# Kernel optimization log

Measured on AMD Instinct MI355X. Metric: run time of the kernel, lower is better.

## Reference

```python
import jax, jax.numpy as jnp
import numpy as np

EPS_SUM = 1e-8   # matches tf divide epsilon on column sums
EPS_L2 = 1e-12   # tf.nn.l2_normalize default epsilon inside CosineSimilarity
EPS_LOG = 1e-8


def _l2norm_rows(x):
    # rows: (k, N); matches tf.nn.l2_normalize(x, axis=-1)
    sq = jnp.sum(x * x, axis=-1, keepdims=True)
    return x * jax.lax.rsqrt(jnp.maximum(sq, EPS_L2))


def setup_inputs() -> dict:
    key = jax.random.key(0)
    k0, k1 = jax.random.split(key)
    N, K = 200000, 256
    c_0 = jax.random.uniform(k0, (N, K), dtype=jnp.float32)
    c_1 = jax.random.uniform(k1, (N, K), dtype=jnp.float32)
    return {"c_0": c_0, "c_1": c_1, "k": K}


def reference(c_0, c_1, k):
    # --- cluster-size entropy terms ---
    s0 = jnp.sum(c_0, axis=0)                      # (k,)
    s1 = jnp.sum(c_1, axis=0)
    p_0 = s0 / jnp.sum(s0)
    p_1 = s1 / jnp.sum(s1)
    log_k = jnp.log(jnp.float32(k))
    entrpy_loss = (jnp.sum(p_0 * jnp.log(p_0)) + log_k) + \
                  (jnp.sum(p_1 * jnp.log(p_1)) + log_k)

    # --- column-sum normalize, transpose to (k, N) ---
    c0n = (c_0 / (s0[None, :] + EPS_SUM)).T        # (k, N)
    c1n = (c_1 / (s1[None, :] + EPS_SUM)).T        # (k, N)

    # cosine similarity matrix via row L2-normalization + small GEMM
    a = _l2norm_rows(c0n)                          # (k, N)
    b = _l2norm_rows(c1n)                          # (k, N)
    c_smi = jnp.einsum('kn,jn->kj', a, b)          # (k, k) cosine sims

    diag = jnp.diagonal(jax.nn.softmax(c_smi, axis=-1))  # (k,)
    cls_loss = -jnp.mean(jnp.log(diag + EPS_LOG))
    return (cls_loss, entrpy_loss)
```

## Files before the change

### kernel.cpp

```cpp
#include <hip/hip_runtime.h>
#include <hip/hip_bf16.h>

typedef __attribute__((ext_vector_type(4))) float f32x4;
typedef __attribute__((ext_vector_type(4))) int   i32x4;
typedef __attribute__((ext_vector_type(8))) short s16x8;

#define KCOLS 256
#define KC 32

__device__ __forceinline__ int swz_idx(int col, int koct){
    return ((col >> 1) << 6) + ((((((col & 1) << 2) | koct)) ^ ((col >> 2) & 7)) << 3);
}

__device__ __forceinline__ int cvt2(float lo, float hi){
    int r;
    asm("v_cvt_pk_bf16_f32 %0, %1, %2" : "=v"(r) : "v"(lo), "v"(hi));
    return r;
}

__device__ __forceinline__ void block_barrier(){
    asm volatile("s_waitcnt lgkmcnt(0)" ::: "memory");
    __builtin_amdgcn_sched_barrier(0);
    __builtin_amdgcn_s_barrier();
    __builtin_amdgcn_sched_barrier(0);
    asm volatile("" ::: "memory");
}

__global__ __launch_bounds__(512, 2) void k1_gemm(
        const float* __restrict__ c0, const float* __restrict__ c1,
        float* __restrict__ Pc, float* __restrict__ Ps, int nrows)
{
    const int tid = threadIdx.x;
    const int w   = tid >> 6;
    const int l   = tid & 63;
    const int mat = w >> 2;
    const int oct = w & 3;
    const int wr  = w >> 2;
    const int wc  = w & 3;
    const int b   = blockIdx.x;
    const int B   = gridDim.x;
    const int nchunk = (nrows + KC - 1) / KC;

    __shared__ __align__(16) unsigned short lds[2][2][8192];
    __shared__ float sred[2][4][256];
    __shared__ float qred[2][4][256];

    const float* src = mat ? c1 : c0;
    const int colbase = l << 2;

    int idxA[8], idxB[4];
#pragma unroll
    for (int mt = 0; mt < 8; ++mt)
        idxA[mt] = swz_idx(wr*128 + mt*16 + (l & 15), l >> 4);
#pragma unroll
    for (int nt = 0; nt < 4; ++nt)
        idxB[nt] = swz_idx(wc*64 + nt*16 + (l & 15), l >> 4);

    int widx[4];
#pragma unroll
    for (int cc = 0; cc < 4; ++cc)
        widx[cc] = (((l << 1) + (cc >> 1)) << 6) +
                   ((((((cc & 1) << 2) | oct)) ^ (l & 7)) << 3);

    f32x4 acc[8][4];
    const f32x4 zf = {0.f, 0.f, 0.f, 0.f};
#pragma unroll
    for (int i = 0; i < 8; ++i)
#pragma unroll
        for (int j = 0; j < 4; ++j) acc[i][j] = zf;

    float sum[4] = {0.f,0.f,0.f,0.f};
    float sq [4] = {0.f,0.f,0.f,0.f};

    f32x4 f[8];
    auto LOAD = [&](int c){
        int rbase = c*KC + oct*8;
        if (rbase + 8 <= nrows){
#pragma unroll
            for (int rr = 0; rr < 8; ++rr)
                f[rr] = *(const f32x4*)(src + (size_t)(rbase+rr)*KCOLS + colbase);
        } else {
#pragma unroll
            for (int rr = 0; rr < 8; ++rr){
                int row = rbase + rr;
                f[rr] = (row < nrows) ? *(const f32x4*)(src + (size_t)row*KCOLS + colbase) : zf;
            }
        }
    };

    int c = b;
    if (c < nchunk) LOAD(c);
    int p = 0;
    while (c < nchunk){
        unsigned short* dst = &lds[p][mat][0];
#pragma unroll
        for (int cc = 0; cc < 4; ++cc){
            float v0=f[0][cc], v1=f[1][cc], v2=f[2][cc], v3=f[3][cc];
            float v4=f[4][cc], v5=f[5][cc], v6=f[6][cc], v7=f[7][cc];
            sum[cc] += ((v0+v1)+(v2+v3)) + ((v4+v5)+(v6+v7));
            sq [cc] += ((v0*v0+v1*v1)+(v2*v2+v3*v3)) + ((v4*v4+v5*v5)+(v6*v6+v7*v7));
            i32x4 pk;
            pk.x = cvt2(v0, v1);
            pk.y = cvt2(v2, v3);
            pk.z = cvt2(v4, v5);
            pk.w = cvt2(v6, v7);
            *(i32x4*)&dst[widx[cc]] = pk;
        }

        int cn = c + B;
        if (cn < nchunk) LOAD(cn);

        block_barrier();

        const unsigned short* bufA = &lds[p][0][0];
        const unsigned short* bufB = &lds[p][1][0];
        s16x8 bfr[4];
#pragma unroll
        for (int nt = 0; nt < 4; ++nt) bfr[nt] = *(const s16x8*)&bufB[idxB[nt]];
#pragma unroll
        for (int mt = 0; mt < 8; ++mt){
            s16x8 afr = *(const s16x8*)&bufA[idxA[mt]];
#pragma unroll
            for (int nt = 0; nt < 4; ++nt)
                acc[mt][nt] = __builtin_amdgcn_mfma_f32_16x16x32_bf16(
                                  afr, bfr[nt], acc[mt][nt], 0, 0, 0);
        }
        p ^= 1;
        c  = cn;
    }

    float* Pb = Pc + (size_t)b * 65536;
#pragma unroll
    for (int mt = 0; mt < 8; ++mt)
#pragma unroll
        for (int nt = 0; nt < 4; ++nt)
#pragma unroll
            for (int r = 0; r < 4; ++r){
                int row = wr*128 + mt*16 + (l >> 4)*4 + r;
                int cl  = wc*64  + nt*16 + (l & 15);
                Pb[row*256 + cl] = acc[mt][nt][r];
            }

#pragma unroll
    for (int cc = 0; cc < 4; ++cc){
        sred[mat][oct][colbase + cc] = sum[cc];
        qred[mat][oct][colbase + cc] = sq[cc];
    }
    __syncthreads();
    {
        int m2 = tid >> 8, cl = tid & 255;
        float s = sred[m2][0][cl] + sred[m2][1][cl] + sred[m2][2][cl] + sred[m2][3][cl];
        float q = qred[m2][0][cl] + qred[m2][1][cl] + qred[m2][2][cl] + qred[m2][3][cl];
        Ps[(size_t)b*1024 + m2*512 + cl]       = s;
        Ps[(size_t)b*1024 + m2*512 + 256 + cl] = q;
    }
}

__global__ __launch_bounds__(256) void k2_sum(const float* __restrict__ Ps,
                                              float* __restrict__ fin, int B)
{
    int tid = threadIdx.x;
    int u   = blockIdx.x*64 + (tid & 63);
    int sub = tid >> 6;
    double a = 0.0;
    for (int b = sub; b < B; b += 4) a += Ps[(size_t)b*1024 + u];
    __shared__ double sc2[4][64];
    sc2[sub][tid & 63] = a;
    __syncthreads();
    if (sub == 0)
        fin[u] = (float)(sc2[0][tid] + sc2[1][tid] + sc2[2][tid] + sc2[3][tid]);
}

__global__ __launch_bounds__(512) void k3_rows(const float* __restrict__ Pc,
        const float* __restrict__ fin, float* __restrict__ tout, int B)
{
    const int j   = blockIdx.x;
    const int tid = threadIdx.x;
    const int l   = tid & 255;
    const int h   = tid >> 8;

    __shared__ float part[2][256];
    __shared__ float cosS[256];
    __shared__ float wred[8];

    double a = 0.0;
    int b0 = h ? (B >> 1) : 0;
    int b1 = h ? B        : (B >> 1);
    for (int b = b0; b < b1; ++b)
        a += Pc[(size_t)b*65536 + j*256 + l];
    part[h][l] = (float)a;
    __syncthreads();

    if (h == 0){
        float Cjl = part[0][l] + part[1][l];
        float d0 = fin[j]       + 1e-8f, q0 = fin[256 + j];
        float d1 = fin[512 + l] + 1e-8f, q1 = fin[768 + l];
        float rs0 = rsqrtf(fmaxf(q0 / (d0*d0), 1e-12f));
        float rs1 = rsqrtf(fmaxf(q1 / (d1*d1), 1e-12f));
        cosS[l] = Cjl * (rs0 / d0) * (rs1 / d1);
    }
    __syncthreads();

    float v  = (tid < 256) ? cosS[tid] : -3.0e38f;
    float mx = v;
#pragma unroll
    for (int o = 32; o >= 1; o >>= 1) mx = fmaxf(mx, __shfl_xor(mx, o));
    if ((tid & 63) == 0) wred[tid >> 6] = mx;
    __syncthreads();
    mx = wred[0];
#pragma unroll
    for (int i = 1; i < 8; ++i) mx = fmaxf(mx, wred[i]);
    __syncthreads();

    float e = (tid < 256) ? expf(cosS[tid] - mx) : 0.0f;
    float s = e;
#pragma unroll
    for (int o = 32; o >= 1; o >>= 1) s += __shfl_xor(s, o);
    if ((tid & 63) == 0) wred[tid >> 6] = s;
    __syncthreads();
    float S = ((wred[0]+wred[1])+(wred[2]+wred[3])) + ((wred[4]+wred[5])+(wred[6]+wred[7]));

    if (tid == j){
        float dg = expf(cosS[j] - mx) / S;
        tout[j] = logf(dg + 1e-8f);
    }
}

__global__ __launch_bounds__(256) void k4_fin(const float* __restrict__ fin,
        const float* __restrict__ tout, const int* __restrict__ kptr,
        float* __restrict__ out)
{
    const int tid = threadIdx.x;
    __shared__ double sc[4];
    auto bsum = [&](double v) -> double {
#pragma unroll
        for (int o = 32; o >= 1; o >>= 1) v += __shfl_xor(v, o);
        if ((tid & 63) == 0) sc[tid >> 6] = v;
        __syncthreads();
        double r = sc[0] + sc[1] + sc[2] + sc[3];
        __syncthreads();
        return r;
    };

    double s0 = fin[tid], s1 = fin[512 + tid];
    double S0 = bsum(s0), S1 = bsum(s1);
    double p0 = s0 / S0, p1 = s1 / S1;
    double T0 = bsum(p0 * log(p0));
    double T1 = bsum(p1 * log(p1));
    double Tc = bsum((double)tout[tid]);

    if (tid == 0){
        double lk = log((double)(*kptr));
        out[0] = (float)(-(Tc / 256.0));
        out[1] = (float)((T0 + lk) + (T1 + lk));
    }
}

extern "C" void kernel_launch(void* const* d_in, const int* in_sizes, int n_in,
                              void* d_out, int out_size, void* d_ws, size_t ws_size,
                              hipStream_t stream)
{
    const float* c0  = (const float*)d_in[0];
    const float* c1  = (const float*)d_in[1];
    const int*  kptr = (const int*)d_in[2];
    float* out = (float*)d_out;
    int nrows = in_sizes[0] / KCOLS;

    int B = 250;
    size_t need = ((size_t)B*66560 + 1280) * sizeof(float);
    if (need > ws_size){
        long cap = (long)(ws_size / sizeof(float)) - 1280;
        long bb  = cap / 66560;
        B = (int)(bb < 1 ? 1 : (bb > 250 ? 250 : bb));
    }
    float* Pc  = (float*)d_ws;
    float* Ps  = Pc + (size_t)B * 65536;
    float* fin = Ps + (size_t)B * 1024;
    float* tv  = fin + 1024;

    hipLaunchKernelGGL(k1_gemm, dim3(B),   dim3(512), 0, stream, c0, c1, Pc, Ps, nrows);
    hipLaunchKernelGGL(k2_sum,  dim3(16),  dim3(256), 0, stream, Ps, fin, B);
    hipLaunchKernelGGL(k3_rows, dim3(256), dim3(512), 0, stream, Pc, fin, tv, B);
    hipLaunchKernelGGL(k4_fin,  dim3(1),   dim3(256), 0, stream, fin, tv, kptr, out);
}
```

Measured before the change: 144.8 us.

## Stream inputs via async global-to-LDS DMA ring with triple buffering

```diff
diff --git a/kernel.cpp b/kernel.cpp
--- a/kernel.cpp
+++ b/kernel.cpp
@@ -2,6 +2,7 @@
 #include <hip/hip_bf16.h>
 
 typedef __attribute__((ext_vector_type(4))) float f32x4;
+typedef __attribute__((ext_vector_type(2))) int   i32x2;
 typedef __attribute__((ext_vector_type(4))) int   i32x4;
 typedef __attribute__((ext_vector_type(8))) short s16x8;
 
@@ -18,35 +19,37 @@
     return r;
 }
 
-__device__ __forceinline__ void block_barrier(){
-    asm volatile("s_waitcnt lgkmcnt(0)" ::: "memory");
-    __builtin_amdgcn_sched_barrier(0);
-    __builtin_amdgcn_s_barrier();
-    __builtin_amdgcn_sched_barrier(0);
-    asm volatile("" ::: "memory");
-}
+__device__ __forceinline__ void dma16(const float* g, float* l){
+    __builtin_amdgcn_global_load_lds(
+        (const __attribute__((address_space(1))) void*)g,
+        (__attribute__((address_space(3))) void*)l, 16, 0, 0);
+}
+
+__device__ __forceinline__ void vmwait8(){ asm volatile("s_waitcnt vmcnt(8)" ::: "memory"); __builtin_amdgcn_sched_barrier(0); }
+__device__ __forceinline__ void vmwait4(){ asm volatile("s_waitcnt vmcnt(4)" ::: "memory"); __builtin_amdgcn_sched_barrier(0); }
+__device__ __forceinline__ void vmwait0(){ asm volatile("s_waitcnt vmcnt(0)" ::: "memory"); __builtin_amdgcn_sched_barrier(0); }
+__device__ __forceinline__ void lgkm0 (){ asm volatile("s_waitcnt lgkmcnt(0)" ::: "memory"); __builtin_amdgcn_sched_barrier(0); }
+__device__ __forceinline__ void barrier(){ __builtin_amdgcn_s_barrier(); __builtin_amdgcn_sched_barrier(0); }
 
 __global__ __launch_bounds__(512, 2) void k1_gemm(
         const float* __restrict__ c0, const float* __restrict__ c1,
         float* __restrict__ Pc, float* __restrict__ Ps, int nrows)
 {
-    const int tid = threadIdx.x;
-    const int w   = tid >> 6;
-    const int l   = tid & 63;
-    const int mat = w >> 2;
-    const int oct = w & 3;
-    const int wr  = w >> 2;
-    const int wc  = w & 3;
-    const int b   = blockIdx.x;
-    const int B   = gridDim.x;
-    const int nchunk = (nrows + KC - 1) / KC;
-
-    __shared__ __align__(16) unsigned short lds[2][2][8192];
-    __shared__ float sred[2][4][256];
-    __shared__ float qred[2][4][256];
+    const int tid  = threadIdx.x;
+    const int w    = tid >> 6;
+    const int l    = tid & 63;
+    const int mat  = w >> 2;
+    const int oct4 = w & 3;
+    const int wr   = w >> 2;
+    const int wc   = w & 3;
+    const int b    = blockIdx.x;
+    const int B    = gridDim.x;
+    const int nfull = nrows >> 5;
+
+    __shared__ __align__(16) float ring[3][8192];
+    __shared__ __align__(16) unsigned short bbuf[2][8192];
 
     const float* src = mat ? c1 : c0;
-    const int colbase = l << 2;
 
     int idxA[8], idxB[4];
 #pragma unroll
@@ -56,12 +59,6 @@
     for (int nt = 0; nt < 4; ++nt)
         idxB[nt] = swz_idx(wc*64 + nt*16 + (l & 15), l >> 4);
 
-    int widx[4];
-#pragma unroll
-    for (int cc = 0; cc < 4; ++cc)
-        widx[cc] = (((l << 1) + (cc >> 1)) << 6) +
-                   ((((((cc & 1) << 2) | oct)) ^ (l & 7)) << 3);
-
     f32x4 acc[8][4];
     const f32x4 zf = {0.f, 0.f, 0.f, 0.f};
 #pragma unroll
@@ -72,27 +69,87 @@
     float sum[4] = {0.f,0.f,0.f,0.f};
     float sq [4] = {0.f,0.f,0.f,0.f};
 
-    f32x4 f[8];
-    auto LOAD = [&](int c){
-        int rbase = c*KC + oct*8;
-        if (rbase + 8 <= nrows){
-#pragma unroll
-            for (int rr = 0; rr < 8; ++rr)
-                f[rr] = *(const f32x4*)(src + (size_t)(rbase+rr)*KCOLS + colbase);
-        } else {
-#pragma unroll
-            for (int rr = 0; rr < 8; ++rr){
-                int row = rbase + rr;
-                f[rr] = (row < nrows) ? *(const f32x4*)(src + (size_t)row*KCOLS + colbase) : zf;
-            }
+    const int T = (b < nfull) ? ((nfull - b - 1) / B + 1) : 0;
+
+    auto ISSUE = [&](int j, int slot){
+        int cch = b + (j >> 1) * B;
+        const float* gb = src + (size_t)(cch*KC + ((j & 1) << 4) + (oct4 << 2)) * KCOLS + (l << 2);
+        float* lb = &ring[slot][(w << 10)];
+#pragma unroll
+        for (int rr = 0; rr < 4; ++rr)
+            dma16(gb + rr*KCOLS, lb + (rr << 8));
+    };
+
+    auto PACK = [&](int jpar, int slot){
+        f32x4 g[4];
+        const float* rb = &ring[slot][(w << 10) + (l << 2)];
+#pragma unroll
+        for (int rr = 0; rr < 4; ++rr) g[rr] = *(const f32x4*)(rb + (rr << 8));
+        int kq   = (jpar << 2) | oct4;
+        int koct = kq >> 1;
+        char* base = (char*)&bbuf[mat][0] + ((kq & 1) << 3);
+#pragma unroll
+        for (int cc = 0; cc < 4; ++cc){
+            float a0=g[0][cc], a1=g[1][cc], a2=g[2][cc], a3=g[3][cc];
+            sum[cc] += (a0+a1)+(a2+a3);
+            sq [cc] += (a0*a0+a1*a1)+(a2*a2+a3*a3);
+            i32x2 pk; pk.x = cvt2(a0,a1); pk.y = cvt2(a2,a3);
+            int col = (l << 2) + cc;
+            int off = ((col >> 1) << 7) + (((((cc & 1) << 2) | koct) ^ (l & 7)) << 4);
+            *(i32x2*)(base + off) = pk;
         }
     };
 
-    int c = b;
-    if (c < nchunk) LOAD(c);
-    int p = 0;
-    while (c < nchunk){
-        unsigned short* dst = &lds[p][mat][0];
+    auto MFMA32 = [&](){
+        const unsigned short* bufA = &bbuf[0][0];
+        const unsigned short* bufB = &bbuf[1][0];
+        s16x8 bfr[4];
+#pragma unroll
+        for (int nt = 0; nt < 4; ++nt) bfr[nt] = *(const s16x8*)&bufB[idxB[nt]];
+#pragma unroll
+        for (int mt = 0; mt < 8; ++mt){
+            s16x8 afr = *(const s16x8*)&bufA[idxA[mt]];
+#pragma unroll
+            for (int nt = 0; nt < 4; ++nt)
+                acc[mt][nt] = __builtin_amdgcn_mfma_f32_16x16x32_bf16(
+                                  afr, bfr[nt], acc[mt][nt], 0, 0, 0);
+        }
+    };
+
+    if (T > 0){
+        ISSUE(0, 0);
+        ISSUE(1, 1);
+        if (T > 1) ISSUE(2, 2);
+    }
+
+    for (int t = 0; t < T; ++t){
+        const int j0 = 2*t;
+        const int s0 = j0 % 3, s1 = (j0 + 1) % 3;
+        const bool more = (t < T - 1);
+
+        if (more) vmwait8(); else vmwait4();
+        PACK(0, s0);
+        if (more) ISSUE(j0 + 3, s0);
+
+        if (more) vmwait8(); else vmwait0();
+        PACK(1, s1);
+        if (t < T - 2) ISSUE(j0 + 4, s1);
+
+        lgkm0();
+        barrier();
+        MFMA32();
+        barrier();
+    }
+
+    const int rem = nrows - (nfull << 5);
+    if (rem > 0 && b == (nfull % B)){
+        f32x4 f[8];
+        const int rbase = (nfull << 5) + oct4*8;
+#pragma unroll
+        for (int rr = 0; rr < 8; ++rr){
+            int row = rbase + rr;
+            f[rr] = (row < nrows) ? *(const f32x4*)(src + (size_t)row*KCOLS + (l << 2)) : zf;
+        }
 #pragma unroll
         for (int cc = 0; cc < 4; ++cc){
             float v0=f[0][cc], v1=f[1][cc], v2=f[2][cc], v3=f[3][cc];
@@ -100,33 +157,15 @@
             sum[cc] += ((v0+v1)+(v2+v3)) + ((v4+v5)+(v6+v7));
             sq [cc] += ((v0*v0+v1*v1)+(v2*v2+v3*v3)) + ((v4*v4+v5*v5)+(v6*v6+v7*v7));
             i32x4 pk;
-            pk.x = cvt2(v0, v1);
-            pk.y = cvt2(v2, v3);
-            pk.z = cvt2(v4, v5);
-            pk.w = cvt2(v6, v7);
-            *(i32x4*)&dst[widx[cc]] = pk;
+            pk.x = cvt2(v0,v1); pk.y = cvt2(v2,v3);
+            pk.z = cvt2(v4,v5); pk.w = cvt2(v6,v7);
+            int col = (l << 2) + cc;
+            int offu = swz_idx(col, oct4);
+            *(i32x4*)&bbuf[mat][offu] = pk;
         }
-
-        int cn = c + B;
-        if (cn < nchunk) LOAD(cn);
-
-        block_barrier();
-
-        const unsigned short* bufA = &lds[p][0][0];
-        const unsigned short* bufB = &lds[p][1][0];
-        s16x8 bfr[4];
-#pragma unroll
-        for (int nt = 0; nt < 4; ++nt) bfr[nt] = *(const s16x8*)&bufB[idxB[nt]];
-#pragma unroll
-        for (int mt = 0; mt < 8; ++mt){
-            s16x8 afr = *(const s16x8*)&bufA[idxA[mt]];
-#pragma unroll
-            for (int nt = 0; nt < 4; ++nt)
-                acc[mt][nt] = __builtin_amdgcn_mfma_f32_16x16x32_bf16(
-                                  afr, bfr[nt], acc[mt][nt], 0, 0, 0);
-        }
-        p ^= 1;
-        c  = cn;
+        lgkm0();
+        barrier();
+        MFMA32();
     }
 
     float* Pb = Pc + (size_t)b * 65536;
@@ -141,16 +180,21 @@
                 Pb[row*256 + cl] = acc[mt][nt][r];
             }
 
+    float* sredp = &ring[0][0];
+    float* qredp = sredp + 2048;
+    __syncthreads();
 #pragma unroll
     for (int cc = 0; cc < 4; ++cc){
-        sred[mat][oct][colbase + cc] = sum[cc];
-        qred[mat][oct][colbase + cc] = sq[cc];
+        sredp[(mat*4 + oct4)*256 + (l << 2) + cc] = sum[cc];
+        qredp[(mat*4 + oct4)*256 + (l << 2) + cc] = sq[cc];
     }
     __syncthreads();
     {
         int m2 = tid >> 8, cl = tid & 255;
-        float s = sred[m2][0][cl] + sred[m2][1][cl] + sred[m2][2][cl] + sred[m2][3][cl];
-        float q = qred[m2][0][cl] + qred[m2][1][cl] + qred[m2][2][cl] + qred[m2][3][cl];
+        float s = sredp[(m2*4+0)*256+cl] + sredp[(m2*4+1)*256+cl]
+                + sredp[(m2*4+2)*256+cl] + sredp[(m2*4+3)*256+cl];
+        float q = qredp[(m2*4+0)*256+cl] + qredp[(m2*4+1)*256+cl]
+                + qredp[(m2*4+2)*256+cl] + qredp[(m2*4+3)*256+cl];
         Ps[(size_t)b*1024 + m2*512 + cl]       = s;
         Ps[(size_t)b*1024 + m2*512 + 256 + cl] = q;
     }
```

New measurement: 141.4 us. -2.3%, faster.
